# Optimization experiments

Hardware: AMD Instinct MI355X
Metric: run time of the kernel (lower is better)

Reference implementation:

```python
import jax, jax.numpy as jnp
import numpy as np


def _gather_neighbors(v, idx):
    # v: [B, N, D], idx: [B, N, K] -> [B, N, K, D]
    return jax.vmap(lambda vb, ib: vb[ib])(v, idx)


def setup_inputs() -> dict:
    key = jax.random.key(0)
    B, N, P, D, K = 8, 2048, 64, 128, 16
    ks = jax.random.split(key, 24)
    s = lambda fan_in: 1.0 / np.sqrt(fan_in)
    inp = {
        "x": jax.random.normal(ks[0], (B, N, 3), jnp.float32),
        "in_f": jax.random.normal(ks[1], (B, N, P), jnp.float32),
        "W_fc1": jax.random.normal(ks[2], (P, D), jnp.float32) * s(P),
        "b_fc1": jnp.zeros((D,), jnp.float32),
        "W_phi": jax.random.normal(ks[3], (D, D), jnp.float32) * s(D),
        "W_psi": jax.random.normal(ks[4], (D, D), jnp.float32) * s(D),
        "W_alpha": jax.random.normal(ks[5], (D, D), jnp.float32) * s(D),
        "W_dpt1": jax.random.normal(ks[6], (D, D), jnp.float32) * s(D),
        "b_dpt1": jnp.zeros((D,), jnp.float32),
        "W_dpt2": jax.random.normal(ks[7], (D, D), jnp.float32) * s(D),
        "b_dpt2": jnp.zeros((D,), jnp.float32),
        "W_gam1": jax.random.normal(ks[8], (D, D), jnp.float32) * s(D),
        "b_gam1": jnp.zeros((D,), jnp.float32),
        "W_gam2": jax.random.normal(ks[9], (D, D), jnp.float32) * s(D),
        "b_gam2": jnp.zeros((D,), jnp.float32),
        "W_del1": jax.random.normal(ks[10], (3, D), jnp.float32) * s(3),
        "b_del1": jnp.zeros((D,), jnp.float32),
        "W_del2": jax.random.normal(ks[11], (D, D), jnp.float32) * s(D),
        "b_del2": jnp.zeros((D,), jnp.float32),
        "W_fc2": jax.random.normal(ks[12], (D, P), jnp.float32) * s(D),
        "b_fc2": jnp.zeros((P,), jnp.float32),
        "k": K,
    }
    return inp


def reference(x, in_f, W_fc1, b_fc1, W_phi, W_psi, W_alpha,
              W_dpt1, b_dpt1, W_dpt2, b_dpt2,
              W_gam1, b_gam1, W_gam2, b_gam2,
              W_del1, b_del1, W_del2, b_del2,
              W_fc2, b_fc2, k):
    # squared pairwise distance [B, N, N] without [B,N,N,3] intermediate
    x2 = jnp.sum(x * x, axis=-1)                      # [B, N]
    d2 = x2[:, :, None] + x2[:, None, :] - 2.0 * jnp.einsum('bnc,bmc->bnm', x, x)
    knn_idx = jnp.argsort(d2, axis=-1)[:, :, :k]       # [B, N, K]

    points_knn = _gather_neighbors(x, knn_idx)         # [B, N, K, 3]
    f = in_f @ W_fc1 + b_fc1                           # [B, N, D]

    # positional encoding delta: MLP(x_i - x_j)
    diff = x[:, :, None, :] - points_knn               # [B, N, K, 3]
    delta = jax.nn.relu(diff @ W_del1 + b_del1) @ W_del2 + b_del2  # [B,N,K,D]

    psi = _gather_neighbors(f @ W_psi, knn_idx)        # [B, N, K, D]
    phi = (f @ W_phi)[:, :, None, :]                   # [B, N, 1, D]
    alpha = _gather_neighbors(f @ W_alpha, knn_idx)    # [B, N, K, D]
    dropped = (jax.nn.relu(f @ W_dpt1 + b_dpt1) @ W_dpt2 + b_dpt2)[:, :, None, :]

    pre = phi - psi + delta + dropped                  # [B, N, K, D]
    gamma = jax.nn.relu(pre @ W_gam1 + b_gam1) @ W_gam2 + b_gam2
    rho = jax.nn.softmax(gamma / jnp.sqrt(jnp.float32(k)), axis=2)

    y = jnp.sum(rho * (alpha + delta), axis=2)         # [B, N, D]
    return y @ W_fc2 + b_fc2 + in_f
```

## Files before the change

### kernel.cpp

```cpp
#include <hip/hip_runtime.h>
#include <hip/hip_bf16.h>
#include <math.h>

#define Bq 8
#define Nq 2048
#define Pq 64
#define Dq 128
#define Kq 16
#define BNq (Bq * Nq)

typedef unsigned short u16;
typedef __bf16 bf16x8v __attribute__((ext_vector_type(8)));
typedef float f32x4v __attribute__((ext_vector_type(4)));

__device__ __forceinline__ u16 f2b(float f) {
    return __builtin_bit_cast(u16, (__bf16)f);
}
__device__ __forceinline__ float b2f(u16 u) {
    return (float)__builtin_bit_cast(__bf16, u);
}

#define OFF_DEL2 0
#define OFF_GAM1 16384
#define OFF_GAM2 32768
#define OFF_FC1  49152
#define OFF_PHI  57344
#define OFF_PSI  73728
#define OFF_ALF  90112
#define OFF_DPT1 106496
#define OFF_DPT2 122880
#define WT_TOTAL 139264

__global__ __launch_bounds__(256) void prep_kernel(
    const float* __restrict__ Wdel2, const float* __restrict__ Wgam1,
    const float* __restrict__ Wgam2, const float* __restrict__ Wfc1,
    const float* __restrict__ Wphi, const float* __restrict__ Wpsi,
    const float* __restrict__ Walpha, const float* __restrict__ Wdpt1,
    const float* __restrict__ Wdpt2, u16* __restrict__ Wt) {
    int idx = blockIdx.x * 256 + threadIdx.x;
    const float* W;
    int n, k;
    if (idx < OFF_FC1) {
        int m = idx >> 14, r = idx & 16383;
        W = (m == 0) ? Wdel2 : (m == 1) ? Wgam1 : Wgam2;
        n = r >> 7; k = r & 127;
    } else if (idx < OFF_PHI) {
        int r = idx - OFF_FC1;
        W = Wfc1; n = r >> 6; k = r & 63;
    } else {
        int r = idx - OFF_PHI;
        int m = r >> 14; r &= 16383;
        W = (m == 0) ? Wphi : (m == 1) ? Wpsi : (m == 2) ? Walpha : (m == 3) ? Wdpt1 : Wdpt2;
        n = r >> 7; k = r & 127;
    }
    Wt[idx] = f2b(W[k * 128 + n]);
}

__global__ __launch_bounds__(256) void knn_kernel(const float* __restrict__ x,
                                                  int* __restrict__ knn) {
    __shared__ float4 sx[Nq];
    __shared__ float sLd[32][8][17];
    __shared__ int   sLi[32][8][17];
    const int b = blockIdx.x >> 6;
    const int q0 = (blockIdx.x & 63) * 32;
    const float* xb = x + b * Nq * 3;
    for (int j = threadIdx.x; j < Nq; j += 256) {
        float x0 = xb[j * 3 + 0], x1 = xb[j * 3 + 1], x2 = xb[j * 3 + 2];
        float n2 = __fadd_rn(__fadd_rn(__fmul_rn(x0, x0), __fmul_rn(x1, x1)),
                             __fmul_rn(x2, x2));
        sx[j] = make_float4(x0, x1, x2, n2);
    }
    __syncthreads();
    const int q = threadIdx.x & 31;
    const int sub = threadIdx.x >> 5;
    const float4 qv = sx[q0 + q];
    float bd[Kq];
    int bj[Kq];
#pragma unroll
    for (int s = 0; s < Kq; ++s) { bd[s] = INFINITY; bj[s] = 0; }
    const int j0 = sub * 256;
    for (int i = 0; i < 256; ++i) {
        const int j = j0 + i;
        float4 p = sx[j];
        float dot = __fadd_rn(__fadd_rn(__fmul_rn(qv.x, p.x), __fmul_rn(qv.y, p.y)),
                              __fmul_rn(qv.z, p.z));
        float d = __fsub_rn(__fadd_rn(qv.w, p.w), __fmul_rn(2.0f, dot));
        if (d < bd[Kq - 1]) {
            bd[Kq - 1] = d; bj[Kq - 1] = j;
#pragma unroll
            for (int s = Kq - 1; s >= 1; --s) {
                if (bd[s] < bd[s - 1]) {
                    float td = bd[s]; bd[s] = bd[s - 1]; bd[s - 1] = td;
                    int tj = bj[s]; bj[s] = bj[s - 1]; bj[s - 1] = tj;
                }
            }
        }
    }
#pragma unroll
    for (int s = 0; s < Kq; ++s) { sLd[q][sub][s] = bd[s]; sLi[q][sub][s] = bj[s]; }
    __syncthreads();
    if (threadIdx.x < 32) {
        const int mq = threadIdx.x;
        int pos[8]; float hd[8]; int hi[8];
#pragma unroll
        for (int s = 0; s < 8; ++s) {
            pos[s] = 1; hd[s] = sLd[mq][s][0]; hi[s] = sLi[mq][s][0];
        }
        int* o = knn + (b * Nq + q0 + mq) * Kq;
#pragma unroll
        for (int oi = 0; oi < Kq; ++oi) {
            float bdv = hd[0]; int biv = hi[0]; int bs = 0;
#pragma unroll
            for (int s = 1; s < 8; ++s) {
                bool take = (hd[s] < bdv) || (hd[s] == bdv && hi[s] < biv);
                if (take) { bdv = hd[s]; biv = hi[s]; bs = s; }
            }
            o[oi] = biv;
#pragma unroll
            for (int s = 0; s < 8; ++s) {
                if (s == bs) {
                    int pp = pos[s] < Kq ? pos[s] : (Kq - 1);
                    bool ok = pos[s] < Kq;
                    hd[s] = ok ? sLd[mq][s][pp] : INFINITY;
                    hi[s] = ok ? sLi[mq][s][pp] : 0x7fffffff;
                    pos[s]++;
                }
            }
        }
    }
}

template <int BYTES, int ROWBYTES>
__device__ __forceinline__ void stageW(const u16* __restrict__ src,
                                       u16* __restrict__ sW, int t) {
#pragma unroll
    for (int c = 0; c < BYTES / 4096; ++c) {
        int lin = c * 4096 + t * 16;
        int n = lin / ROWBYTES;
        int o = lin % ROWBYTES;
        bf16x8v v = *(const bf16x8v*)((const char*)src + lin);
        *(bf16x8v*)((char*)sW + n * ROWBYTES + (o ^ ((n & 7) << 4))) = v;
    }
}

__device__ __forceinline__ void mfma_k128(const u16* __restrict__ sA,
                                          const u16* __restrict__ sW,
                                          int colbase, int lane,
                                          f32x4v (&acc)[4][2]) {
    const int kg = lane >> 4;
    const int l15 = lane & 15;
#pragma unroll
    for (int ks = 0; ks < 4; ++ks) {
        bf16x8v a[4], bfr[2];
#pragma unroll
        for (int m = 0; m < 4; ++m) {
            int row = m * 16 + l15;
            int o = (ks * 64 + kg * 16) ^ ((row & 7) << 4);
            a[m] = *(const bf16x8v*)((const char*)sA + row * 256 + o);
        }
#pragma unroll
        for (int nt = 0; nt < 2; ++nt) {
            int n = colbase + nt * 16 + l15;
            int o = (ks * 64 + kg * 16) ^ ((n & 7) << 4);
            bfr[nt] = *(const bf16x8v*)((const char*)sW + n * 256 + o);
        }
#pragma unroll
        for (int m = 0; m < 4; ++m)
#pragma unroll
            for (int nt = 0; nt < 2; ++nt)
                acc[m][nt] = __builtin_amdgcn_mfma_f32_16x16x32_bf16(a[m], bfr[nt], acc[m][nt], 0, 0, 0);
    }
}

__device__ __forceinline__ void mfma_k64(const u16* __restrict__ sA,
                                         const u16* __restrict__ sW,
                                         int colbase, int lane,
                                         f32x4v (&acc)[4][2]) {
    const int kg = lane >> 4;
    const int l15 = lane & 15;
#pragma unroll
    for (int ks = 0; ks < 2; ++ks) {
        bf16x8v a[4], bfr[2];
#pragma unroll
        for (int m = 0; m < 4; ++m) {
            int row = m * 16 + l15;
            int o = (ks * 64 + kg * 16) ^ ((row & 7) << 4);
            a[m] = *(const bf16x8v*)((const char*)sA + row * 128 + o);
        }
#pragma unroll
        for (int nt = 0; nt < 2; ++nt) {
            int n = colbase + nt * 16 + l15;
            int o = (ks * 64 + kg * 16) ^ ((n & 7) << 4);
            bfr[nt] = *(const bf16x8v*)((const char*)sW + n * 128 + o);
        }
#pragma unroll
        for (int m = 0; m < 4; ++m)
#pragma unroll
            for (int nt = 0; nt < 2; ++nt)
                acc[m][nt] = __builtin_amdgcn_mfma_f32_16x16x32_bf16(a[m], bfr[nt], acc[m][nt], 0, 0, 0);
    }
}

__global__ __launch_bounds__(256, 2) void feat_kernel(
    const float* __restrict__ in_f, const u16* __restrict__ Wt,
    const float* __restrict__ bfc1, const float* __restrict__ bdpt1,
    const float* __restrict__ bdpt2,
    float* __restrict__ base, u16* __restrict__ psiB, u16* __restrict__ alphaB) {
    __shared__ __align__(16) u16 sIn[64 * 64];
    __shared__ __align__(16) u16 sF[64 * 128];
    __shared__ __align__(16) u16 sW[128 * 128];
    const int t = threadIdx.x;
    const int lane = t & 63;
    const int w = t >> 6;
    const int kg = lane >> 4;
    const int l15 = lane & 15;
    const int p0 = blockIdx.x * 64;

    {
        const int r = t >> 2;
        const int c0 = (t & 3) * 16;
        const float* src = &in_f[(size_t)(p0 + r) * 64 + c0];
        float4 v0 = *(const float4*)(src + 0);
        float4 v1 = *(const float4*)(src + 4);
        float4 v2 = *(const float4*)(src + 8);
        float4 v3 = *(const float4*)(src + 12);
        bf16x8v lo, hi;
        lo[0] = (__bf16)v0.x; lo[1] = (__bf16)v0.y; lo[2] = (__bf16)v0.z; lo[3] = (__bf16)v0.w;
        lo[4] = (__bf16)v1.x; lo[5] = (__bf16)v1.y; lo[6] = (__bf16)v1.z; lo[7] = (__bf16)v1.w;
        hi[0] = (__bf16)v2.x; hi[1] = (__bf16)v2.y; hi[2] = (__bf16)v2.z; hi[3] = (__bf16)v2.w;
        hi[4] = (__bf16)v3.x; hi[5] = (__bf16)v3.y; hi[6] = (__bf16)v3.z; hi[7] = (__bf16)v3.w;
        const int swz = (r & 7) << 4;
        *(bf16x8v*)((char*)sIn + r * 128 + ((c0 * 2) ^ swz)) = lo;
        *(bf16x8v*)((char*)sIn + r * 128 + (((c0 + 8) * 2) ^ swz)) = hi;
    }

    f32x4v acc[4][2], accPhi[4][2];

    {
        float bv0 = bfc1[w * 32 + l15];
        float bv1 = bfc1[w * 32 + 16 + l15];
#pragma unroll
        for (int m = 0; m < 4; ++m) { acc[m][0] = f32x4v{bv0, bv0, bv0, bv0}; acc[m][1] = f32x4v{bv1, bv1, bv1, bv1}; }
    }
    stageW<16384, 128>(Wt + OFF_FC1, sW, t);
    __syncthreads();
    mfma_k64(sIn, sW, w * 32, lane, acc);

#pragma unroll
    for (int m = 0; m < 4; ++m)
#pragma unroll
        for (int nt = 0; nt < 2; ++nt)
#pragma unroll
            for (int rr = 0; rr < 4; ++rr) {
                int row = m * 16 + kg * 4 + rr;
                int col = w * 32 + nt * 16 + l15;
                *(__bf16*)((char*)sF + row * 256 + ((col * 2) ^ ((row & 7) << 4))) = (__bf16)acc[m][nt][rr];
            }

#pragma unroll
    for (int m = 0; m < 4; ++m) { accPhi[m][0] = f32x4v{0, 0, 0, 0}; accPhi[m][1] = f32x4v{0, 0, 0, 0}; }
    __syncthreads();
    stageW<32768, 256>(Wt + OFF_PHI, sW, t);
    __syncthreads();
    mfma_k128(sF, sW, w * 32, lane, accPhi);

#pragma unroll
    for (int m = 0; m < 4; ++m) { acc[m][0] = f32x4v{0, 0, 0, 0}; acc[m][1] = f32x4v{0, 0, 0, 0}; }
    __syncthreads();
    stageW<32768, 256>(Wt + OFF_PSI, sW, t);
    __syncthreads();
    mfma_k128(sF, sW, w * 32, lane, acc);
#pragma unroll
    for (int m = 0; m < 4; ++m)
#pragma unroll
        for (int nt = 0; nt < 2; ++nt)
#pragma unroll
            for (int rr = 0; rr < 4; ++rr) {
                int row = m * 16 + kg * 4 + rr;
                int col = w * 32 + nt * 16 + l15;
                psiB[(size_t)(p0 + row) * 128 + col] = f2b(acc[m][nt][rr]);
            }

#pragma unroll
    for (int m = 0; m < 4; ++m) { acc[m][0] = f32x4v{0, 0, 0, 0}; acc[m][1] = f32x4v{0, 0, 0, 0}; }
    __syncthreads();
    stageW<32768, 256>(Wt + OFF_ALF, sW, t);
    __syncthreads();
    mfma_k128(sF, sW, w * 32, lane, acc);
#pragma unroll
    for (int m = 0; m < 4; ++m)
#pragma unroll
        for (int nt = 0; nt < 2; ++nt)
#pragma unroll
            for (int rr = 0; rr < 4; ++rr) {
                int row = m * 16 + kg * 4 + rr;
                int col = w * 32 + nt * 16 + l15;
                alphaB[(size_t)(p0 + row) * 128 + col] = f2b(acc[m][nt][rr]);
            }

    {
        float bv0 = bdpt1[w * 32 + l15];
        float bv1 = bdpt1[w * 32 + 16 + l15];
#pragma unroll
        for (int m = 0; m < 4; ++m) { acc[m][0] = f32x4v{bv0, bv0, bv0, bv0}; acc[m][1] = f32x4v{bv1, bv1, bv1, bv1}; }
    }
    __syncthreads();
    stageW<32768, 256>(Wt + OFF_DPT1, sW, t);
    __syncthreads();
    mfma_k128(sF, sW, w * 32, lane, acc);
    __syncthreads();
#pragma unroll
    for (int m = 0; m < 4; ++m)
#pragma unroll
        for (int nt = 0; nt < 2; ++nt)
#pragma unroll
            for (int rr = 0; rr < 4; ++rr) {
                int row = m * 16 + kg * 4 + rr;
                int col = w * 32 + nt * 16 + l15;
                *(__bf16*)((char*)sF + row * 256 + ((col * 2) ^ ((row & 7) << 4))) =
                    (__bf16)fmaxf(acc[m][nt][rr], 0.f);
            }

    {
        float bv0 = bdpt2[w * 32 + l15];
        float bv1 = bdpt2[w * 32 + 16 + l15];
#pragma unroll
        for (int m = 0; m < 4; ++m) { acc[m][0] = f32x4v{bv0, bv0, bv0, bv0}; acc[m][1] = f32x4v{bv1, bv1, bv1, bv1}; }
    }
    __syncthreads();
    stageW<32768, 256>(Wt + OFF_DPT2, sW, t);
    __syncthreads();
    mfma_k128(sF, sW, w * 32, lane, acc);
#pragma unroll
    for (int m = 0; m < 4; ++m)
#pragma unroll
        for (int nt = 0; nt < 2; ++nt)
#pragma unroll
            for (int rr = 0; rr < 4; ++rr) {
                int row = m * 16 + kg * 4 + rr;
                int col = w * 32 + nt * 16 + l15;
                base[(size_t)(p0 + row) * 128 + col] = acc[m][nt][rr] + accPhi[m][nt][rr];
            }
}

__device__ __forceinline__ void mfma_ldsB(const u16* __restrict__ sA,
                                          const u16* __restrict__ sW,
                                          int colW, int kg, int l15,
                                          f32x4v (&acc)[4]) {
#pragma unroll
    for (int ks = 0; ks < 4; ++ks) {
        bf16x8v a[4], bb;
#pragma unroll
        for (int m = 0; m < 4; ++m) {
            int row = m * 16 + l15;
            int o = (ks * 64 + kg * 16) ^ ((row & 7) << 4);
            a[m] = *(const bf16x8v*)((const char*)sA + row * 256 + o);
        }
        {
            int o = (ks * 64 + kg * 16) ^ ((colW & 7) << 4);
            bb = *(const bf16x8v*)((const char*)sW + colW * 256 + o);
        }
#pragma unroll
        for (int m = 0; m < 4; ++m)
            acc[m] = __builtin_amdgcn_mfma_f32_16x16x32_bf16(a[m], bb, acc[m], 0, 0, 0);
    }
}

__device__ __forceinline__ void mfma_regB(const u16* __restrict__ sA,
                                          const bf16x8v (&wB)[4],
                                          int kg, int l15,
                                          f32x4v (&acc)[4]) {
#pragma unroll
    for (int ks = 0; ks < 4; ++ks) {
#pragma unroll
        for (int m = 0; m < 4; ++m) {
            int row = m * 16 + l15;
            int o = (ks * 64 + kg * 16) ^ ((row & 7) << 4);
            bf16x8v a = *(const bf16x8v*)((const char*)sA + row * 256 + o);
            acc[m] = __builtin_amdgcn_mfma_f32_16x16x32_bf16(a, wB[ks], acc[m], 0, 0, 0);
        }
    }
}

__global__ __launch_bounds__(512, 4) void main_kernel(
    const float* __restrict__ x, const float* __restrict__ in_f,
    const float* __restrict__ Wdel1, const float* __restrict__ bdel1,
    const float* __restrict__ bdel2,
    const float* __restrict__ bgam1, const float* __restrict__ bgam2,
    const float* __restrict__ Wfc2, const float* __restrict__ bfc2,
    const float* __restrict__ base, const u16* __restrict__ psiB,
    const u16* __restrict__ alphaB, const int* __restrict__ knn,
    const u16* __restrict__ Wt, float* __restrict__ out) {
    __shared__ __align__(16) u16 sWd2[128 * 128];
    __shared__ __align__(16) u16 sA[64 * 128];
    __shared__ float sWd1[512];
    __shared__ int sIdx[64];
    __shared__ float sY[4][128];

    const int t = threadIdx.x;
    const int lane = t & 63;
    const int w = t >> 6;
    const int kg = lane >> 4;
    const int l15 = lane & 15;
    const int colW = w * 16 + l15;

#pragma unroll
    for (int c = 0; c < 4; ++c) {
        int lin = c * 8192 + t * 16;
        int n = lin >> 8;
        int o = lin & 255;
        bf16x8v v = *(const bf16x8v*)((const char*)(Wt + OFF_DEL2) + lin);
        *(bf16x8v*)((char*)sWd2 + n * 256 + (o ^ ((n & 7) << 4))) = v;
    }
    {
        int idx = t;
        if (idx < 512) sWd1[idx] = (idx < 384) ? Wdel1[idx] : bdel1[idx - 384];
    }
    bf16x8v wG1[4], wG2[4];
#pragma unroll
    for (int ks = 0; ks < 4; ++ks) {
        size_t off = (size_t)colW * 128 + ks * 32 + kg * 8;
        wG1[ks] = *(const bf16x8v*)(Wt + OFF_GAM1 + off);
        wG2[ks] = *(const bf16x8v*)(Wt + OFF_GAM2 + off);
    }
    const float bD = bdel2[colW];
    const float bG1 = bgam1[colW];
    const float bG2 = bgam2[colW];
    float bO = 0.f;
    if (t < 256) bO = bfc2[t & 63];

    const int pbase = blockIdx.x * 16;
    const int b = pbase >> 11;
    const int hr = t >> 3;
    const int hc0 = (t & 7) * 16;

    for (int chunk = 0; chunk < 4; ++chunk) {
        const int p0 = pbase + chunk * 4;

        if (t < 64) {
            int p = p0 + (t >> 4);
            sIdx[t] = b * Nq + knn[p * Kq + (t & 15)];
        }

        {
            const int p = p0 + (hr >> 4);
            const int j = knn[p * Kq + (hr & 15)];
            const float* xq = x + (size_t)p * 3;
            const float* xn = x + (size_t)(b * Nq + j) * 3;
            const float dx = xq[0] - xn[0];
            const float dy = xq[1] - xn[1];
            const float dz = xq[2] - xn[2];
            const int swzB = (hr & 7) << 4;
#pragma unroll
            for (int hh = 0; hh < 2; ++hh) {
                bf16x8v hv;
#pragma unroll
                for (int c4 = 0; c4 < 2; ++c4) {
                    const int cc = hc0 + hh * 8 + c4 * 4;
                    float4 wx = *(const float4*)&sWd1[cc];
                    float4 wy = *(const float4*)&sWd1[128 + cc];
                    float4 wz = *(const float4*)&sWd1[256 + cc];
                    float4 b4 = *(const float4*)&sWd1[384 + cc];
                    hv[c4 * 4 + 0] = (__bf16)fmaxf(fmaf(dz, wz.x, fmaf(dy, wy.x, fmaf(dx, wx.x, b4.x))), 0.f);
                    hv[c4 * 4 + 1] = (__bf16)fmaxf(fmaf(dz, wz.y, fmaf(dy, wy.y, fmaf(dx, wx.y, b4.y))), 0.f);
                    hv[c4 * 4 + 2] = (__bf16)fmaxf(fmaf(dz, wz.z, fmaf(dy, wy.z, fmaf(dx, wx.z, b4.z))), 0.f);
                    hv[c4 * 4 + 3] = (__bf16)fmaxf(fmaf(dz, wz.w, fmaf(dy, wy.w, fmaf(dx, wx.w, b4.w))), 0.f);
                }
                *(bf16x8v*)((char*)sA + hr * 256 + (((hc0 + hh * 8) * 2) ^ swzB)) = hv;
            }
        }
        __syncthreads();

        f32x4v accD[4];
#pragma unroll
        for (int m = 0; m < 4; ++m) accD[m] = f32x4v{bD, bD, bD, bD};
        mfma_ldsB(sA, sWd2, colW, kg, l15, accD);
        __syncthreads();

#pragma unroll
        for (int m = 0; m < 4; ++m) {
            const float bs = base[(size_t)(p0 + m) * 128 + colW];
#pragma unroll
            for (int rr = 0; rr < 4; ++rr) {
                int row = m * 16 + kg * 4 + rr;
                float ps = b2f(psiB[(size_t)sIdx[row] * 128 + colW]);
                int off = row * 256 + ((colW * 2) ^ ((row & 7) << 4));
                *(__bf16*)((char*)sA + off) = (__bf16)(accD[m][rr] + (bs - ps));
            }
        }
        __syncthreads();

        f32x4v accT[4];
#pragma unroll
        for (int m = 0; m < 4; ++m) accT[m] = f32x4v{bG1, bG1, bG1, bG1};
        mfma_regB(sA, wG1, kg, l15, accT);
        __syncthreads();

#pragma unroll
        for (int m = 0; m < 4; ++m)
#pragma unroll
            for (int rr = 0; rr < 4; ++rr) {
                int row = m * 16 + kg * 4 + rr;
                int off = row * 256 + ((colW * 2) ^ ((row & 7) << 4));
                *(__bf16*)((char*)sA + off) = (__bf16)fmaxf(accT[m][rr], 0.f);
            }
        __syncthreads();

#pragma unroll
        for (int m = 0; m < 4; ++m) accT[m] = f32x4v{bG2, bG2, bG2, bG2};
        mfma_regB(sA, wG2, kg, l15, accT);

#pragma unroll
        for (int m = 0; m < 4; ++m) {
            float g0 = accT[m][0], g1v = accT[m][1], g2 = accT[m][2], g3 = accT[m][3];
            float mx = fmaxf(fmaxf(g0, g1v), fmaxf(g2, g3));
            mx = fmaxf(mx, __shfl_xor(mx, 16, 64));
            mx = fmaxf(mx, __shfl_xor(mx, 32, 64));
            float m4 = mx * 0.25f;
            float e0 = expf(0.25f * g0 - m4), e1 = expf(0.25f * g1v - m4);
            float e2 = expf(0.25f * g2 - m4), e3 = expf(0.25f * g3 - m4);
            float s = e0 + e1 + e2 + e3;
            s += __shfl_xor(s, 16, 64);
            s += __shfl_xor(s, 32, 64);
            float y = 0.f;
#pragma unroll
            for (int rr = 0; rr < 4; ++rr) {
                int row = m * 16 + kg * 4 + rr;
                float al = b2f(alphaB[(size_t)sIdx[row] * 128 + colW]);
                float ev = (rr == 0) ? e0 : (rr == 1) ? e1 : (rr == 2) ? e2 : e3;
                y = fmaf(ev, al + accD[m][rr], y);
            }
            y += __shfl_xor(y, 16, 64);
            y += __shfl_xor(y, 32, 64);
            if (kg == 0) sY[m][colW] = y / s;
        }
        __syncthreads();

        if (t < 256) {
            const int p = t >> 6;
            const int q = t & 63;
            const int gp = p0 + p;
            float a = bO + in_f[(size_t)gp * 64 + q];
#pragma unroll 8
            for (int d = 0; d < 128; ++d)
                a = fmaf(sY[p][d], Wfc2[d * 64 + q], a);
            out[(size_t)gp * 64 + q] = a;
        }
    }
}

extern "C" void kernel_launch(void* const* d_in, const int* in_sizes, int n_in,
                              void* d_out, int out_size, void* d_ws, size_t ws_size,
                              hipStream_t stream) {
    const float* x     = (const float*)d_in[0];
    const float* in_f  = (const float*)d_in[1];
    const float* Wfc1  = (const float*)d_in[2];
    const float* bfc1  = (const float*)d_in[3];
    const float* Wphi  = (const float*)d_in[4];
    const float* Wpsi  = (const float*)d_in[5];
    const float* Walpha= (const float*)d_in[6];
    const float* Wdpt1 = (const float*)d_in[7];
    const float* bdpt1 = (const float*)d_in[8];
    const float* Wdpt2 = (const float*)d_in[9];
    const float* bdpt2 = (const float*)d_in[10];
    const float* Wgam1 = (const float*)d_in[11];
    const float* bgam1 = (const float*)d_in[12];
    const float* Wgam2 = (const float*)d_in[13];
    const float* bgam2 = (const float*)d_in[14];
    const float* Wdel1 = (const float*)d_in[15];
    const float* bdel1 = (const float*)d_in[16];
    const float* Wdel2 = (const float*)d_in[17];
    const float* bdel2 = (const float*)d_in[18];
    const float* Wfc2  = (const float*)d_in[19];
    const float* bfc2  = (const float*)d_in[20];
    float* out = (float*)d_out;

    float* base   = (float*)d_ws;
    u16*   psiB   = (u16*)(base + (size_t)BNq * Dq);
    u16*   alphaB = psiB + (size_t)BNq * Dq;
    int*   knn    = (int*)(alphaB + (size_t)BNq * Dq);
    u16*   Wt     = (u16*)(knn + (size_t)BNq * Kq);

    prep_kernel<<<WT_TOTAL / 256, 256, 0, stream>>>(Wdel2, Wgam1, Wgam2, Wfc1, Wphi,
                                                    Wpsi, Walpha, Wdpt1, Wdpt2, Wt);
    knn_kernel<<<512, 256, 0, stream>>>(x, knn);
    feat_kernel<<<BNq / 64, 256, 0, stream>>>(in_f, Wt, bfc1, bdpt1, bdpt2,
                                              base, psiB, alphaB);
    main_kernel<<<BNq / 16, 512, 0, stream>>>(x, in_f, Wdel1, bdel1, bdel2,
                                              bgam1, bgam2, Wfc2, bfc2,
                                              base, psiB, alphaB, knn, Wt, out);
}
```

Measured before the change: 254.2 us.

## Double-buffer LDS tile, prefetch gathers into registers, cut barriers in main kernel

Uses two ping-pong sA buffers so fewer __syncthreads are needed per chunk, replacing them with a lightweight lgkmcnt-wait barrier. Psi/alpha gathers and the next chunk's knn/x coordinates are loaded into registers early, so their global latency overlaps MFMA work, and the shared sIdx array is removed. The final fc2 projection is split across all 512 threads, each summing half of the reduction and combining via shuffle. This adds register pressure under launch_bounds(512,4) and makes the barrier semantics more delicate.

New measurement: 396.7 us. 56.1% more time.

```diff
diff --git a/kernel.cpp b/kernel.cpp
--- a/kernel.cpp
+++ b/kernel.cpp
@@ -19,6 +19,10 @@
 __device__ __forceinline__ float b2f(u16 u) {
     return (float)__builtin_bit_cast(__bf16, u);
 }
+
+#define BARRIER() do { asm volatile("s_waitcnt lgkmcnt(0)" ::: "memory"); \
+                       __builtin_amdgcn_s_barrier();                       \
+                       __builtin_amdgcn_sched_barrier(0); } while (0)
 
 #define OFF_DEL2 0
 #define OFF_GAM1 16384
@@ -392,9 +396,8 @@
     const u16* __restrict__ alphaB, const int* __restrict__ knn,
     const u16* __restrict__ Wt, float* __restrict__ out) {
     __shared__ __align__(16) u16 sWd2[128 * 128];
-    __shared__ __align__(16) u16 sA[64 * 128];
+    __shared__ __align__(16) u16 sA[2][64 * 128];
     __shared__ float sWd1[512];
-    __shared__ int sIdx[64];
     __shared__ float sY[4][128];
 
     const int t = threadIdx.x;
@@ -404,6 +407,21 @@
     const int l15 = lane & 15;
     const int colW = w * 16 + l15;
 
+    const int pbase = blockIdx.x * 16;
+    const int b = pbase >> 11;
+    const int bN = b * Nq;
+    const int hr = t >> 3;
+    const int hc0 = (t & 7) * 16;
+
+    int pB = pbase + (hr >> 4);
+    int jB = knn[pB * Kq + (hr & 15)];
+    float cxq0 = x[(size_t)pB * 3 + 0];
+    float cxq1 = x[(size_t)pB * 3 + 1];
+    float cxq2 = x[(size_t)pB * 3 + 2];
+    float cxn0 = x[(size_t)(bN + jB) * 3 + 0];
+    float cxn1 = x[(size_t)(bN + jB) * 3 + 1];
+    float cxn2 = x[(size_t)(bN + jB) * 3 + 2];
+
 #pragma unroll
     for (int c = 0; c < 4; ++c) {
         int lin = c * 8192 + t * 16;
@@ -412,10 +430,7 @@
         bf16x8v v = *(const bf16x8v*)((const char*)(Wt + OFF_DEL2) + lin);
         *(bf16x8v*)((char*)sWd2 + n * 256 + (o ^ ((n & 7) << 4))) = v;
     }
-    {
-        int idx = t;
-        if (idx < 512) sWd1[idx] = (idx < 384) ? Wdel1[idx] : bdel1[idx - 384];
-    }
+    sWd1[t] = (t < 384) ? Wdel1[t] : bdel1[t - 384];
     bf16x8v wG1[4], wG2[4];
 #pragma unroll
     for (int ks = 0; ks < 4; ++ks) {
@@ -426,30 +441,18 @@
     const float bD = bdel2[colW];
     const float bG1 = bgam1[colW];
     const float bG2 = bgam2[colW];
-    float bO = 0.f;
-    if (t < 256) bO = bfc2[t & 63];
-
-    const int pbase = blockIdx.x * 16;
-    const int b = pbase >> 11;
-    const int hr = t >> 3;
-    const int hc0 = (t & 7) * 16;
-
-    for (int chunk = 0; chunk < 4; ++chunk) {
-        const int p0 = pbase + chunk * 4;
-
-        if (t < 64) {
-            int p = p0 + (t >> 4);
-            sIdx[t] = b * Nq + knn[p * Kq + (t & 15)];
-        }
+    const float bOq = bfc2[(t & 127) >> 1];
+    __syncthreads();
+
+    for (int c = 0; c < 4; ++c) {
+        const int p0 = pbase + c * 4;
+        u16* sAh = sA[c & 1];
+        u16* sAp = sA[1 - (c & 1)];
 
         {
-            const int p = p0 + (hr >> 4);
-            const int j = knn[p * Kq + (hr & 15)];
-            const float* xq = x + (size_t)p * 3;
-            const float* xn = x + (size_t)(b * Nq + j) * 3;
-            const float dx = xq[0] - xn[0];
-            const float dy = xq[1] - xn[1];
-            const float dz = xq[2] - xn[2];
+            const float dx = cxq0 - cxn0;
+            const float dy = cxq1 - cxn1;
+            const float dz = cxq2 - cxn2;
             const int swzB = (hr & 7) << 4;
 #pragma unroll
             for (int hh = 0; hh < 2; ++hh) {
@@ -466,35 +469,30 @@
                     hv[c4 * 4 + 2] = (__bf16)fmaxf(fmaf(dz, wz.z, fmaf(dy, wy.z, fmaf(dx, wx.z, b4.z))), 0.f);
                     hv[c4 * 4 + 3] = (__bf16)fmaxf(fmaf(dz, wz.w, fmaf(dy, wy.w, fmaf(dx, wx.w, b4.w))), 0.f);
                 }
-                *(bf16x8v*)((char*)sA + hr * 256 + (((hc0 + hh * 8) * 2) ^ swzB)) = hv;
-            }
-        }
-        __syncthreads();
+                *(bf16x8v*)((char*)sAh + hr * 256 + (((hc0 + hh * 8) * 2) ^ swzB)) = hv;
+            }
+        }
+
+        int4 ivv[4];
+#pragma unroll
+        for (int m = 0; m < 4; ++m)
+            ivv[m] = *(const int4*)&knn[(p0 + m) * Kq + kg * 4];
+        u16 ps[4][4];
+        float bs[4];
+#pragma unroll
+        for (int m = 0; m < 4; ++m) {
+            bs[m] = base[(size_t)(p0 + m) * 128 + colW];
+            const int ii[4] = {ivv[m].x, ivv[m].y, ivv[m].z, ivv[m].w};
+#pragma unroll
+            for (int rr = 0; rr < 4; ++rr)
+                ps[m][rr] = psiB[(size_t)(bN + ii[rr]) * 128 + colW];
+        }
+        BARRIER();
 
         f32x4v accD[4];
 #pragma unroll
         for (int m = 0; m < 4; ++m) accD[m] = f32x4v{bD, bD, bD, bD};
-        mfma_ldsB(sA, sWd2, colW, kg, l15, accD);
-        __syncthreads();
-
-#pragma unroll
-        for (int m = 0; m < 4; ++m) {
-            const float bs = base[(size_t)(p0 + m) * 128 + colW];
-#pragma unroll
-            for (int rr = 0; rr < 4; ++rr) {
-                int row = m * 16 + kg * 4 + rr;
-                float ps = b2f(psiB[(size_t)sIdx[row] * 128 + colW]);
-                int off = row * 256 + ((colW * 2) ^ ((row & 7) << 4));
-                *(__bf16*)((char*)sA + off) = (__bf16)(accD[m][rr] + (bs - ps));
-            }
-        }
-        __syncthreads();
-
-        f32x4v accT[4];
-#pragma unroll
-        for (int m = 0; m < 4; ++m) accT[m] = f32x4v{bG1, bG1, bG1, bG1};
-        mfma_regB(sA, wG1, kg, l15, accT);
-        __syncthreads();
+        mfma_ldsB(sAh, sWd2, colW, kg, l15, accD);
 
 #pragma unroll
         for (int m = 0; m < 4; ++m)
@@ -502,13 +500,40 @@
             for (int rr = 0; rr < 4; ++rr) {
                 int row = m * 16 + kg * 4 + rr;
                 int off = row * 256 + ((colW * 2) ^ ((row & 7) << 4));
-                *(__bf16*)((char*)sA + off) = (__bf16)fmaxf(accT[m][rr], 0.f);
-            }
-        __syncthreads();
+                *(__bf16*)((char*)sAp + off) = (__bf16)(accD[m][rr] + (bs[m] - b2f(ps[m][rr])));
+            }
+
+        u16 al[4][4];
+#pragma unroll
+        for (int m = 0; m < 4; ++m) {
+            const int ii[4] = {ivv[m].x, ivv[m].y, ivv[m].z, ivv[m].w};
+#pragma unroll
+            for (int rr = 0; rr < 4; ++rr)
+                al[m][rr] = alphaB[(size_t)(bN + ii[rr]) * 128 + colW];
+        }
+        BARRIER();
+
+        f32x4v accT[4];
+#pragma unroll
+        for (int m = 0; m < 4; ++m) accT[m] = f32x4v{bG1, bG1, bG1, bG1};
+        mfma_regB(sAp, wG1, kg, l15, accT);
+#pragma unroll
+        for (int m = 0; m < 4; ++m)
+#pragma unroll
+            for (int rr = 0; rr < 4; ++rr) {
+                int row = m * 16 + kg * 4 + rr;
+                int off = row * 256 + ((colW * 2) ^ ((row & 7) << 4));
+                *(__bf16*)((char*)sAh + off) = (__bf16)fmaxf(accT[m][rr], 0.f);
+            }
+        BARRIER();
 
 #pragma unroll
         for (int m = 0; m < 4; ++m) accT[m] = f32x4v{bG2, bG2, bG2, bG2};
-        mfma_regB(sA, wG2, kg, l15, accT);
+        mfma_regB(sAh, wG2, kg, l15, accT);
+
+        const int pN = pbase + (c + 1) * 4 + (hr >> 4);
+        int jN = 0;
+        if (c < 3) jN = knn[pN * Kq + (hr & 15)];
 
 #pragma unroll
         for (int m = 0; m < 4; ++m) {
@@ -522,29 +547,38 @@
             float s = e0 + e1 + e2 + e3;
             s += __shfl_xor(s, 16, 64);
             s += __shfl_xor(s, 32, 64);
-            float y = 0.f;
-#pragma unroll
-            for (int rr = 0; rr < 4; ++rr) {
-                int row = m * 16 + kg * 4 + rr;
-                float al = b2f(alphaB[(size_t)sIdx[row] * 128 + colW]);
-                float ev = (rr == 0) ? e0 : (rr == 1) ? e1 : (rr == 2) ? e2 : e3;
-                y = fmaf(ev, al + accD[m][rr], y);
-            }
+            float y = fmaf(e0, b2f(al[m][0]) + accD[m][0],
+                      fmaf(e1, b2f(al[m][1]) + accD[m][1],
+                      fmaf(e2, b2f(al[m][2]) + accD[m][2],
+                           e3 * (b2f(al[m][3]) + accD[m][3]))));
             y += __shfl_xor(y, 16, 64);
             y += __shfl_xor(y, 32, 64);
             if (kg == 0) sY[m][colW] = y / s;
         }
-        __syncthreads();
-
-        if (t < 256) {
-            const int p = t >> 6;
-            const int q = t & 63;
+        BARRIER();
+
+        {
+            const int p = t >> 7;
+            const int q = (t & 127) >> 1;
+            const int half = t & 1;
             const int gp = p0 + p;
-            float a = bO + in_f[(size_t)gp * 64 + q];
-#pragma unroll 8
-            for (int d = 0; d < 128; ++d)
-                a = fmaf(sY[p][d], Wfc2[d * 64 + q], a);
-            out[(size_t)gp * 64 + q] = a;
+            float a = 0.f;
+            const float* wcol = Wfc2 + (half * 64) * 64 + q;
+#pragma unroll 16
+            for (int d = 0; d < 64; ++d)
+                a = fmaf(sY[p][half * 64 + d], wcol[d * 64], a);
+            a += __shfl_xor(a, 1, 64);
+            if (half == 0)
+                out[(size_t)gp * 64 + q] = a + bOq + in_f[(size_t)gp * 64 + q];
+        }
+
+        if (c < 3) {
+            cxq0 = x[(size_t)pN * 3 + 0];
+            cxq1 = x[(size_t)pN * 3 + 1];
+            cxq2 = x[(size_t)pN * 3 + 2];
+            cxn0 = x[(size_t)(bN + jN) * 3 + 0];
+            cxn1 = x[(size_t)(bN + jN) * 3 + 1];
+            cxn2 = x[(size_t)(bN + jN) * 3 + 2];
         }
     }
 }
```

## Fold gamma1 weights into delta, phi, psi and dropped projections algebraically

Applied to the files above, without the earlier changes.

Because pre feeds a linear layer before its ReLU, W_gam1 is pre-multiplied into W_del2, W_phi, W_psi and W_dpt2 on device, and the biases are folded into one effective bias. The main kernel then runs the gamma1 MFMA directly on the delta hidden activations, alongside the delta MFMA, which removes one LDS round trip and two barriers per chunk. The base and psi intermediates are stored as bf16 to halve their traffic, and the final fc2 projection now uses all 512 threads with a shuffle reduction. Pre-multiplying the weights in fp32 and rounding once to bf16 changes the rounding behaviour, and the extra small prep kernels add launch overhead.

Result: slower. 336.2 us (+32.2%).

```diff
diff --git a/kernel.cpp b/kernel.cpp
--- a/kernel.cpp
+++ b/kernel.cpp
@@ -31,29 +31,67 @@
 #define OFF_DPT2 122880
 #define WT_TOTAL 139264
 
-__global__ __launch_bounds__(256) void prep_kernel(
-    const float* __restrict__ Wdel2, const float* __restrict__ Wgam1,
-    const float* __restrict__ Wgam2, const float* __restrict__ Wfc1,
-    const float* __restrict__ Wphi, const float* __restrict__ Wpsi,
-    const float* __restrict__ Walpha, const float* __restrict__ Wdpt1,
-    const float* __restrict__ Wdpt2, u16* __restrict__ Wt) {
+__global__ __launch_bounds__(256) void prep_direct(
+    const float* __restrict__ Wdel2, const float* __restrict__ Wgam2,
+    const float* __restrict__ Wfc1, const float* __restrict__ Walpha,
+    const float* __restrict__ Wdpt1, u16* __restrict__ Wt) {
     int idx = blockIdx.x * 256 + threadIdx.x;
-    const float* W;
-    int n, k;
-    if (idx < OFF_FC1) {
-        int m = idx >> 14, r = idx & 16383;
-        W = (m == 0) ? Wdel2 : (m == 1) ? Wgam1 : Wgam2;
-        n = r >> 7; k = r & 127;
-    } else if (idx < OFF_PHI) {
-        int r = idx - OFF_FC1;
-        W = Wfc1; n = r >> 6; k = r & 63;
-    } else {
-        int r = idx - OFF_PHI;
-        int m = r >> 14; r &= 16383;
-        W = (m == 0) ? Wphi : (m == 1) ? Wpsi : (m == 2) ? Walpha : (m == 3) ? Wdpt1 : Wdpt2;
-        n = r >> 7; k = r & 127;
-    }
-    Wt[idx] = f2b(W[k * 128 + n]);
+    if (idx < 16384) {
+        int n = idx >> 7, k = idx & 127;
+        Wt[OFF_DEL2 + idx] = f2b(Wdel2[k * 128 + n]);
+    } else if (idx < 32768) {
+        int r = idx - 16384, n = r >> 7, k = r & 127;
+        Wt[OFF_GAM2 + r] = f2b(Wgam2[k * 128 + n]);
+    } else if (idx < 40960) {
+        int r = idx - 32768, n = r >> 6, k = r & 63;
+        Wt[OFF_FC1 + r] = f2b(Wfc1[k * 128 + n]);
+    } else if (idx < 57344) {
+        int r = idx - 40960, n = r >> 7, k = r & 127;
+        Wt[OFF_ALF + r] = f2b(Walpha[k * 128 + n]);
+    } else if (idx < 73728) {
+        int r = idx - 57344, n = r >> 7, k = r & 127;
+        Wt[OFF_DPT1 + r] = f2b(Wdpt1[k * 128 + n]);
+    }
+}
+
+__global__ __launch_bounds__(256) void prep_mm(
+    const float* __restrict__ Wdel2, const float* __restrict__ Wphi,
+    const float* __restrict__ Wpsi, const float* __restrict__ Wdpt2,
+    const float* __restrict__ Wgam1, u16* __restrict__ Wt) {
+    __shared__ float sB[128 * 128];
+    for (int i = threadIdx.x; i < 16384; i += 256) sB[i] = Wgam1[i];
+    __syncthreads();
+    const int mat = blockIdx.x >> 3;
+    const int chunk = blockIdx.x & 7;
+    const float* A = (mat == 0) ? Wdel2 : (mat == 1) ? Wphi : (mat == 2) ? Wpsi : Wdpt2;
+    const int OFF = (mat == 0) ? OFF_GAM1 : (mat == 1) ? OFF_PHI : (mat == 2) ? OFF_PSI : OFF_DPT2;
+    const int o0 = chunk * 2048 + threadIdx.x * 8;
+    const int n = o0 >> 7, k0 = o0 & 127;
+#pragma unroll
+    for (int kk = 0; kk < 8; ++kk) {
+        const float* Ar = A + (size_t)(k0 + kk) * 128;
+        float s = 0.f;
+        for (int j = 0; j < 128; j += 4) {
+            float4 a4 = *(const float4*)(Ar + j);
+            s = fmaf(a4.x, sB[(j + 0) * 128 + n], s);
+            s = fmaf(a4.y, sB[(j + 1) * 128 + n], s);
+            s = fmaf(a4.z, sB[(j + 2) * 128 + n], s);
+            s = fmaf(a4.w, sB[(j + 3) * 128 + n], s);
+        }
+        Wt[OFF + n * 128 + k0 + kk] = f2b(s);
+    }
+}
+
+__global__ void prep_bias(const float* __restrict__ bgam1,
+                          const float* __restrict__ bdel2,
+                          const float* __restrict__ bdpt2,
+                          const float* __restrict__ Wgam1,
+                          float* __restrict__ bGt) {
+    int n = threadIdx.x;
+    float s = bgam1[n];
+    for (int k = 0; k < 128; ++k)
+        s = fmaf(bdel2[k] + bdpt2[k], Wgam1[k * 128 + n], s);
+    bGt[n] = s;
 }
 
 __global__ __launch_bounds__(256) void knn_kernel(const float* __restrict__ x,
@@ -204,8 +242,7 @@
 __global__ __launch_bounds__(256, 2) void feat_kernel(
     const float* __restrict__ in_f, const u16* __restrict__ Wt,
     const float* __restrict__ bfc1, const float* __restrict__ bdpt1,
-    const float* __restrict__ bdpt2,
-    float* __restrict__ base, u16* __restrict__ psiB, u16* __restrict__ alphaB) {
+    u16* __restrict__ baseGB, u16* __restrict__ psiGB, u16* __restrict__ alphaB) {
     __shared__ __align__(16) u16 sIn[64 * 64];
     __shared__ __align__(16) u16 sF[64 * 128];
     __shared__ __align__(16) u16 sW[128 * 128];
@@ -278,7 +315,7 @@
             for (int rr = 0; rr < 4; ++rr) {
                 int row = m * 16 + kg * 4 + rr;
                 int col = w * 32 + nt * 16 + l15;
-                psiB[(size_t)(p0 + row) * 128 + col] = f2b(acc[m][nt][rr]);
+                psiGB[(size_t)(p0 + row) * 128 + col] = f2b(acc[m][nt][rr]);
             }
 
 #pragma unroll
@@ -321,12 +358,8 @@
                     (__bf16)fmaxf(acc[m][nt][rr], 0.f);
             }
 
-    {
-        float bv0 = bdpt2[w * 32 + l15];
-        float bv1 = bdpt2[w * 32 + 16 + l15];
-#pragma unroll
-        for (int m = 0; m < 4; ++m) { acc[m][0] = f32x4v{bv0, bv0, bv0, bv0}; acc[m][1] = f32x4v{bv1, bv1, bv1, bv1}; }
-    }
+#pragma unroll
+    for (int m = 0; m < 4; ++m) { acc[m][0] = f32x4v{0, 0, 0, 0}; acc[m][1] = f32x4v{0, 0, 0, 0}; }
     __syncthreads();
     stageW<32768, 256>(Wt + OFF_DPT2, sW, t);
     __syncthreads();
@@ -339,56 +372,17 @@
             for (int rr = 0; rr < 4; ++rr) {
                 int row = m * 16 + kg * 4 + rr;
                 int col = w * 32 + nt * 16 + l15;
-                base[(size_t)(p0 + row) * 128 + col] = acc[m][nt][rr] + accPhi[m][nt][rr];
-            }
-}
-
-__device__ __forceinline__ void mfma_ldsB(const u16* __restrict__ sA,
-                                          const u16* __restrict__ sW,
-                                          int colW, int kg, int l15,
-                                          f32x4v (&acc)[4]) {
-#pragma unroll
-    for (int ks = 0; ks < 4; ++ks) {
-        bf16x8v a[4], bb;
-#pragma unroll
-        for (int m = 0; m < 4; ++m) {
-            int row = m * 16 + l15;
-            int o = (ks * 64 + kg * 16) ^ ((row & 7) << 4);
-            a[m] = *(const bf16x8v*)((const char*)sA + row * 256 + o);
-        }
-        {
-            int o = (ks * 64 + kg * 16) ^ ((colW & 7) << 4);
-            bb = *(const bf16x8v*)((const char*)sW + colW * 256 + o);
-        }
-#pragma unroll
-        for (int m = 0; m < 4; ++m)
-            acc[m] = __builtin_amdgcn_mfma_f32_16x16x32_bf16(a[m], bb, acc[m], 0, 0, 0);
-    }
-}
-
-__device__ __forceinline__ void mfma_regB(const u16* __restrict__ sA,
-                                          const bf16x8v (&wB)[4],
-                                          int kg, int l15,
-                                          f32x4v (&acc)[4]) {
-#pragma unroll
-    for (int ks = 0; ks < 4; ++ks) {
-#pragma unroll
-        for (int m = 0; m < 4; ++m) {
-            int row = m * 16 + l15;
-            int o = (ks * 64 + kg * 16) ^ ((row & 7) << 4);
-            bf16x8v a = *(const bf16x8v*)((const char*)sA + row * 256 + o);
-            acc[m] = __builtin_amdgcn_mfma_f32_16x16x32_bf16(a, wB[ks], acc[m], 0, 0, 0);
-        }
-    }
+                baseGB[(size_t)(p0 + row) * 128 + col] = f2b(acc[m][nt][rr] + accPhi[m][nt][rr]);
+            }
 }
 
 __global__ __launch_bounds__(512, 4) void main_kernel(
     const float* __restrict__ x, const float* __restrict__ in_f,
     const float* __restrict__ Wdel1, const float* __restrict__ bdel1,
-    const float* __restrict__ bdel2,
-    const float* __restrict__ bgam1, const float* __restrict__ bgam2,
+    const float* __restrict__ bdel2, const float* __restrict__ bGt,
+    const float* __restrict__ bgam2,
     const float* __restrict__ Wfc2, const float* __restrict__ bfc2,
-    const float* __restrict__ base, const u16* __restrict__ psiB,
+    const u16* __restrict__ baseGB, const u16* __restrict__ psiGB,
     const u16* __restrict__ alphaB, const int* __restrict__ knn,
     const u16* __restrict__ Wt, float* __restrict__ out) {
     __shared__ __align__(16) u16 sWd2[128 * 128];
@@ -404,6 +398,12 @@
     const int l15 = lane & 15;
     const int colW = w * 16 + l15;
 
+    const int pbase = blockIdx.x * 16;
+    const int b = pbase >> 11;
+    const int bN = b * Nq;
+    const int hr = t >> 3;
+    const int hc0 = (t & 7) * 16;
+
 #pragma unroll
     for (int c = 0; c < 4; ++c) {
         int lin = c * 8192 + t * 16;
@@ -412,10 +412,7 @@
         bf16x8v v = *(const bf16x8v*)((const char*)(Wt + OFF_DEL2) + lin);
         *(bf16x8v*)((char*)sWd2 + n * 256 + (o ^ ((n & 7) << 4))) = v;
     }
-    {
-        int idx = t;
-        if (idx < 512) sWd1[idx] = (idx < 384) ? Wdel1[idx] : bdel1[idx - 384];
-    }
+    sWd1[t] = (t < 384) ? Wdel1[t] : bdel1[t - 384];
     bf16x8v wG1[4], wG2[4];
 #pragma unroll
     for (int ks = 0; ks < 4; ++ks) {
@@ -424,29 +421,24 @@
         wG2[ks] = *(const bf16x8v*)(Wt + OFF_GAM2 + off);
     }
     const float bD = bdel2[colW];
-    const float bG1 = bgam1[colW];
+    const float bG1 = bGt[colW];
     const float bG2 = bgam2[colW];
-    float bO = 0.f;
-    if (t < 256) bO = bfc2[t & 63];
-
-    const int pbase = blockIdx.x * 16;
-    const int b = pbase >> 11;
-    const int hr = t >> 3;
-    const int hc0 = (t & 7) * 16;
-
-    for (int chunk = 0; chunk < 4; ++chunk) {
-        const int p0 = pbase + chunk * 4;
+    const float bOq = bfc2[(t & 127) >> 1];
+    __syncthreads();
+
+    for (int c = 0; c < 4; ++c) {
+        const int p0 = pbase + c * 4;
 
         if (t < 64) {
             int p = p0 + (t >> 4);
-            sIdx[t] = b * Nq + knn[p * Kq + (t & 15)];
+            sIdx[t] = bN + knn[p * Kq + (t & 15)];
         }
 
         {
             const int p = p0 + (hr >> 4);
             const int j = knn[p * Kq + (hr & 15)];
             const float* xq = x + (size_t)p * 3;
-            const float* xn = x + (size_t)(b * Nq + j) * 3;
+            const float* xn = x + (size_t)(bN + j) * 3;
             const float dx = xq[0] - xn[0];
             const float dy = xq[1] - xn[1];
             const float dz = xq[2] - xn[2];
@@ -471,44 +463,53 @@
         }
         __syncthreads();
 
-        f32x4v accD[4];
-#pragma unroll
-        for (int m = 0; m < 4; ++m) accD[m] = f32x4v{bD, bD, bD, bD};
-        mfma_ldsB(sA, sWd2, colW, kg, l15, accD);
+        f32x4v accD[4], accG[4];
+#pragma unroll
+        for (int m = 0; m < 4; ++m) { accD[m] = f32x4v{bD, bD, bD, bD}; accG[m] = f32x4v{bG1, bG1, bG1, bG1}; }
+#pragma unroll
+        for (int ks = 0; ks < 4; ++ks) {
+            bf16x8v bbD;
+            {
+                int o = (ks * 64 + kg * 16) ^ ((colW & 7) << 4);
+                bbD = *(const bf16x8v*)((const char*)sWd2 + colW * 256 + o);
+            }
+#pragma unroll
+            for (int m = 0; m < 4; ++m) {
+                int row = m * 16 + l15;
+                int o = (ks * 64 + kg * 16) ^ ((row & 7) << 4);
+                bf16x8v a = *(const bf16x8v*)((const char*)sA + row * 256 + o);
+                accD[m] = __builtin_amdgcn_mfma_f32_16x16x32_bf16(a, bbD, accD[m], 0, 0, 0);
+                accG[m] = __builtin_amdgcn_mfma_f32_16x16x32_bf16(a, wG1[ks], accG[m], 0, 0, 0);
+            }
+        }
         __syncthreads();
 
 #pragma unroll
         for (int m = 0; m < 4; ++m) {
-            const float bs = base[(size_t)(p0 + m) * 128 + colW];
-#pragma unroll
-            for (int rr = 0; rr < 4; ++rr) {
-                int row = m * 16 + kg * 4 + rr;
-                float ps = b2f(psiB[(size_t)sIdx[row] * 128 + colW]);
+            const float bsf = b2f(baseGB[(size_t)(p0 + m) * 128 + colW]);
+#pragma unroll
+            for (int rr = 0; rr < 4; ++rr) {
+                int row = m * 16 + kg * 4 + rr;
+                float ps = b2f(psiGB[(size_t)sIdx[row] * 128 + colW]);
                 int off = row * 256 + ((colW * 2) ^ ((row & 7) << 4));
-                *(__bf16*)((char*)sA + off) = (__bf16)(accD[m][rr] + (bs - ps));
+                *(__bf16*)((char*)sA + off) = (__bf16)fmaxf(accG[m][rr] + (bsf - ps), 0.f);
             }
         }
         __syncthreads();
 
         f32x4v accT[4];
 #pragma unroll
-        for (int m = 0; m < 4; ++m) accT[m] = f32x4v{bG1, bG1, bG1, bG1};
-        mfma_regB(sA, wG1, kg, l15, accT);
-        __syncthreads();
-
-#pragma unroll
-        for (int m = 0; m < 4; ++m)
-#pragma unroll
-            for (int rr = 0; rr < 4; ++rr) {
-                int row = m * 16 + kg * 4 + rr;
-                int off = row * 256 + ((colW * 2) ^ ((row & 7) << 4));
-                *(__bf16*)((char*)sA + off) = (__bf16)fmaxf(accT[m][rr], 0.f);
-            }
-        __syncthreads();
-
-#pragma unroll
         for (int m = 0; m < 4; ++m) accT[m] = f32x4v{bG2, bG2, bG2, bG2};
-        mfma_regB(sA, wG2, kg, l15, accT);
+#pragma unroll
+        for (int ks = 0; ks < 4; ++ks) {
+#pragma unroll
+            for (int m = 0; m < 4; ++m) {
+                int row = m * 16 + l15;
+                int o = (ks * 64 + kg * 16) ^ ((row & 7) << 4);
+                bf16x8v a = *(const bf16x8v*)((const char*)sA + row * 256 + o);
+                accT[m] = __builtin_amdgcn_mfma_f32_16x16x32_bf16(a, wG2[ks], accT[m], 0, 0, 0);
+            }
+        }
 
 #pragma unroll
         for (int m = 0; m < 4; ++m) {
@@ -536,15 +537,19 @@
         }
         __syncthreads();
 
-        if (t < 256) {
-            const int p = t >> 6;
-            const int q = t & 63;
+        {
+            const int p = t >> 7;
+            const int q = (t & 127) >> 1;
+            const int half = t & 1;
             const int gp = p0 + p;
-            float a = bO + in_f[(size_t)gp * 64 + q];
-#pragma unroll 8
-            for (int d = 0; d < 128; ++d)
-                a = fmaf(sY[p][d], Wfc2[d * 64 + q], a);
-            out[(size_t)gp * 64 + q] = a;
+            float a = 0.f;
+            const float* wcol = Wfc2 + (half * 64) * 64 + q;
+#pragma unroll 16
+            for (int d = 0; d < 64; ++d)
+                a = fmaf(sY[p][half * 64 + d], wcol[d * 64], a);
+            a += __shfl_xor(a, 1, 64);
+            if (half == 0)
+                out[(size_t)gp * 64 + q] = a + bOq + in_f[(size_t)gp * 64 + q];
         }
     }
 }
@@ -575,18 +580,20 @@
     const float* bfc2  = (const float*)d_in[20];
     float* out = (float*)d_out;
 
-    float* base   = (float*)d_ws;
-    u16*   psiB   = (u16*)(base + (size_t)BNq * Dq);
-    u16*   alphaB = psiB + (size_t)BNq * Dq;
+    u16*   baseGB = (u16*)d_ws;
+    u16*   psiGB  = baseGB + (size_t)BNq * Dq;
+    u16*   alphaB = psiGB + (size_t)BNq * Dq;
     int*   knn    = (int*)(alphaB + (size_t)BNq * Dq);
     u16*   Wt     = (u16*)(knn + (size_t)BNq * Kq);
-
-    prep_kernel<<<WT_TOTAL / 256, 256, 0, stream>>>(Wdel2, Wgam1, Wgam2, Wfc1, Wphi,
-                                                    Wpsi, Walpha, Wdpt1, Wdpt2, Wt);
+    float* bGt    = (float*)(Wt + WT_TOTAL);
+
+    prep_direct<<<288, 256, 0, stream>>>(Wdel2, Wgam2, Wfc1, Walpha, Wdpt1, Wt);
+    prep_mm<<<32, 256, 0, stream>>>(Wdel2, Wphi, Wpsi, Wdpt2, Wgam1, Wt);
+    prep_bias<<<1, 128, 0, stream>>>(bgam1, bdel2, bdpt2, Wgam1, bGt);
     knn_kernel<<<512, 256, 0, stream>>>(x, knn);
-    feat_kernel<<<BNq / 64, 256, 0, stream>>>(in_f, Wt, bfc1, bdpt1, bdpt2,
-                                              base, psiB, alphaB);
-    main_kernel<<<BNq / 16, 512, 0, stream>>>(x, in_f, Wdel1, bdel1, bdel2,
-                                              bgam1, bgam2, Wfc2, bfc2,
-                                              base, psiB, alphaB, knn, Wt, out);
-}
+    feat_kernel<<<BNq / 64, 256, 0, stream>>>(in_f, Wt, bfc1, bdpt1,
+                                              baseGB, psiGB, alphaB);
+    main_kernel<<<BNq / 16, 512, 0, stream>>>(x, in_f, Wdel1, bdel1, bdel2, bGt,
+                                              bgam2, Wfc2, bfc2,
+                                              baseGB, psiGB, alphaB, knn, Wt, out);
+}
```
